# Kernel tuning notes

Measured on AMD Instinct MI355X. Metric: run time of the kernel, lower is better.

The kernel has to match this reference:

```python
import jax, jax.numpy as jnp
import numpy as np

B = 4096
NC = 64        # n_concepts
NT = 16        # n_tasks
H = 256        # prior_units (prior_layers = 1)
HID = 256      # prior_hids = [256, 256]
K = 20         # n_components
IN = 3 * NC + NT + 1        # GRU input size = 209
MLP_IN = H + 3 * NC + NT    # rnn_out input = 464
LOG_2PI = float(np.log(2.0 * np.pi))


def setup_inputs() -> dict:
    key = jax.random.key(0)
    ks = jax.random.split(key, 16)
    s = 0.05
    inp = {
        "z": jax.random.normal(ks[0], (B, NC), jnp.float32),
        "c": jax.random.normal(ks[1], (B, NC + NT), jnp.float32),
        "b": (jax.random.uniform(ks[2], (B, NC)) < 0.5).astype(jnp.float32),
        "m": (jax.random.uniform(ks[3], (B, NC)) < 0.5).astype(jnp.float32),
        # GRU (PyTorch layout: gates ordered r, z, n)
        "W_ih": jax.random.normal(ks[4], (3 * H, IN), jnp.float32) * s,
        "W_hh": jax.random.normal(ks[5], (3 * H, H), jnp.float32) * s,
        "b_ih": jax.random.normal(ks[6], (3 * H,), jnp.float32) * s,
        "b_hh": jax.random.normal(ks[7], (3 * H,), jnp.float32) * s,
        # rnn_out MLP: Linear(464,256)+Tanh, Linear(256,256)+Tanh, Linear(256,3K)
        "W1": jax.random.normal(ks[8], (HID, MLP_IN), jnp.float32) * s,
        "b1": jax.random.normal(ks[9], (HID,), jnp.float32) * s,
        "W2": jax.random.normal(ks[10], (HID, HID), jnp.float32) * s,
        "b2": jax.random.normal(ks[11], (HID,), jnp.float32) * s,
        "W3": jax.random.normal(ks[12], (3 * K, HID), jnp.float32) * s,
        "b3": jax.random.normal(ks[13], (3 * K,), jnp.float32) * s,
    }
    return inp


def _logp(z, c, b, m, W_ih, W_hh, b_ih, b_hh, W1, b1, W2, b2, W3, b3):
    Bsz, d = z.shape
    cbm = jnp.concatenate([c, b, m], axis=1)               # [B, 3*NC+NT]
    # z input at step t is -1 for t=0, else z[:, t-1]
    z_prev = jnp.concatenate(
        [-jnp.ones((Bsz, 1), z.dtype), z[:, :-1]], axis=1)  # [B, d]
    # Precompute the input-gate projections for all steps without
    # materializing the full [d, B, IN] sequence tensor:
    # column 0 of W_ih multiplies z_prev; the rest multiplies cbm.
    gi_cbm = cbm @ W_ih[:, 1:].T + b_ih                    # [B, 3H]
    gi = gi_cbm[None, :, :] + z_prev.T[:, :, None] * W_ih[:, 0][None, None, :]  # [d, B, 3H]

    def gru_step(h, gi_t):
        gh = h @ W_hh.T + b_hh
        gi_r, gi_u, gi_n = jnp.split(gi_t, 3, axis=-1)
        gh_r, gh_u, gh_n = jnp.split(gh, 3, axis=-1)
        r = jax.nn.sigmoid(gi_r + gh_r)
        u = jax.nn.sigmoid(gi_u + gh_u)
        n = jnp.tanh(gi_n + r * gh_n)
        h_new = (1.0 - u) * n + u * h
        return h_new, h_new

    h0 = jnp.zeros((Bsz, W_hh.shape[1]), z.dtype)
    _, hs = jax.lax.scan(gru_step, h0, gi)                 # [d, B, H]
    hs = jnp.transpose(hs, (1, 0, 2))                      # [B, d, H]

    feat = jnp.concatenate(
        [hs, jnp.broadcast_to(cbm[:, None, :], (Bsz, d, cbm.shape[1]))],
        axis=2)                                            # [B, d, MLP_IN]
    h1 = jnp.tanh(feat @ W1.T + b1)
    h2 = jnp.tanh(h1 @ W2.T + b2)
    params = h2 @ W3.T + b3                                # [B, d, 3K]

    logits, means, lsigmas = jnp.split(params, 3, axis=-1)
    t = z[..., None]                                       # [B, d, 1]
    log_norm = -lsigmas - 0.5 * LOG_2PI
    diff = (t - means) * jnp.exp(-lsigmas)
    log_kernel = -0.5 * jnp.square(diff)
    log_like = (jax.nn.logsumexp(log_kernel + log_norm + logits, axis=-1)
                - jax.nn.logsumexp(logits, axis=-1))       # [B, d]

    query = m * (1.0 - b)
    mask = jnp.sort(query, axis=1)[:, ::-1]                # descending sort of values
    return jnp.sum(log_like * mask, axis=1)                # [B]


def reference(z, c, b, m, W_ih, W_hh, b_ih, b_hh, W1, b1, W2, b2, W3, b3):
    return _logp(z, c, b, m, W_ih, W_hh, b_ih, b_hh,
                 W1, b1, W2, b2, W3, b3)
```

## Files before the change

kernel.cpp:

```cpp
#include <hip/hip_runtime.h>
#include <hip/hip_bf16.h>

#define BATCH  4096
#define NCC    64
#define HDIM   256
#define G3     768
#define NROW   (BATCH*NCC)
#define NK     20
#define LOG2PI 1.8378770664093453f

typedef __attribute__((ext_vector_type(8))) short bf16x8;
typedef __attribute__((ext_vector_type(4))) float f32x4;

__device__ __forceinline__ float sigm(float x) { return 1.0f/(1.0f + __expf(-x)); }
__device__ __forceinline__ float tanh_fast(float x) { return 1.0f - 2.0f/(__expf(2.0f*x) + 1.0f); }
__device__ __forceinline__ unsigned short f2bf(float x) {
  __hip_bfloat16 h = __float2bfloat16(x);
  return __builtin_bit_cast(unsigned short, h);
}

__global__ __launch_bounds__(256) void k_cvtall(
    const float* __restrict__ c, const float* __restrict__ bv,
    const float* __restrict__ mv, const float* __restrict__ W_ih,
    const float* __restrict__ W_hh, const float* __restrict__ W1,
    const float* __restrict__ W2, const float* __restrict__ W3,
    unsigned short* __restrict__ cbmB, unsigned short* __restrict__ CW,
    unsigned short* __restrict__ WhhB, unsigned short* __restrict__ W1aB,
    unsigned short* __restrict__ W2B, unsigned short* __restrict__ W3pB,
    float* __restrict__ w0) {
  int idx = blockIdx.x*256 + threadIdx.x;
  if (idx < 1048576) {
    int row = idx >> 8, k = idx & 255;
    float v = 0.f;
    if (k < 80)       v = c [row*80 + k];
    else if (k < 144) v = bv[row*64 + (k-80)];
    else if (k < 208) v = mv[row*64 + (k-144)];
    cbmB[idx] = f2bf(v);
    return;
  }
  idx -= 1048576;
  if (idx < 262144) {
    int n = idx >> 8, k = idx & 255;
    float v = 0.f;
    if (n < 768) { if (k < 208) v = W_ih[n*209 + 1 + k]; }
    else         { if (k < 208) v = W1[(n-768)*464 + 256 + k]; }
    CW[idx] = f2bf(v);
    return;
  }
  idx -= 262144;
  if (idx < 196608) { WhhB[idx] = f2bf(W_hh[idx]); return; }
  idx -= 196608;
  if (idx < 65536) { int n = idx>>8, k = idx&255; W1aB[idx] = f2bf(W1[n*464+k]); return; }
  idx -= 65536;
  if (idx < 65536) { W2B[idx] = f2bf(W2[idx]); return; }
  idx -= 65536;
  if (idx < 16384) {
    int n = idx >> 8;
    float v = 0.f;
    if (n < 60) v = W3[idx];
    W3pB[idx] = f2bf(v);
    return;
  }
  idx -= 16384;
  if (idx < 768) w0[idx] = W_ih[idx*209];
}

__global__ __launch_bounds__(512) void k_pre(
    const unsigned short* __restrict__ A, const unsigned short* __restrict__ Bw,
    const float* __restrict__ b_ih, const float* __restrict__ b_hh,
    const float* __restrict__ b1,
    float* __restrict__ gi, float* __restrict__ P1) {
  __shared__ __align__(16) unsigned short As[128*64];
  __shared__ __align__(16) unsigned short Bs[128*64];
  int tid = threadIdx.x;
  int rb = blockIdx.x >> 3, cb = blockIdx.x & 7;
  long row0 = (long)rb * 128;
  int n0 = cb * 128;
  int wv = tid >> 6, lane = tid & 63;
  int lq = lane >> 4, l16 = lane & 15;
  int wrg = wv & 3, wcg = wv >> 2;
  f32x4 acc[2][4];
#pragma unroll
  for (int i = 0; i < 2; ++i)
#pragma unroll
    for (int j = 0; j < 4; ++j) acc[i][j] = (f32x4){0.f,0.f,0.f,0.f};
  for (int kb = 0; kb < 256; kb += 64) {
#pragma unroll
    for (int i = 0; i < 2; ++i) {
      int s = i*512 + tid;
      int r = s >> 3, cg = (s & 7) ^ (r & 7);
      *(uint4*)&As[s*8] = *(const uint4*)&A[(row0 + r)*256 + kb + cg*8];
      *(uint4*)&Bs[s*8] = *(const uint4*)&Bw[(long)(n0 + r)*256 + kb + cg*8];
    }
    __syncthreads();
#pragma unroll
    for (int kc = 0; kc < 2; ++kc) {
      int csel = kc*4 + lq;
      bf16x8 af[2];
#pragma unroll
      for (int rt = 0; rt < 2; ++rt) {
        int r = wrg*32 + rt*16 + l16;
        af[rt] = *(const bf16x8*)&As[r*64 + ((csel ^ (r & 7)))*8];
      }
#pragma unroll
      for (int ct = 0; ct < 4; ++ct) {
        int n = wcg*64 + ct*16 + l16;
        bf16x8 bfr = *(const bf16x8*)&Bs[n*64 + ((csel ^ (n & 7)))*8];
        acc[0][ct] = __builtin_amdgcn_mfma_f32_16x16x32_bf16(af[0], bfr, acc[0][ct], 0, 0, 0);
        acc[1][ct] = __builtin_amdgcn_mfma_f32_16x16x32_bf16(af[1], bfr, acc[1][ct], 0, 0, 0);
      }
    }
    __syncthreads();
  }
#pragma unroll
  for (int rt = 0; rt < 2; ++rt)
#pragma unroll
    for (int q = 0; q < 4; ++q) {
      long row = row0 + wrg*32 + rt*16 + lq*4 + q;
#pragma unroll
      for (int ct = 0; ct < 4; ++ct) {
        int n = n0 + wcg*64 + ct*16 + l16;
        float v = acc[rt][ct][q];
        if (n < 512)      gi[row*G3 + n] = v + b_ih[n] + b_hh[n];
        else if (n < 768) gi[row*G3 + n] = v + b_ih[n];
        else              P1[row*256 + (n-768)] = v + b1[n-768];
      }
    }
}

__global__ __launch_bounds__(512, 2) void k_gru(
    const float* __restrict__ z, const float* __restrict__ gi,
    const unsigned short* __restrict__ WhhB, const float* __restrict__ b_hh,
    const float* __restrict__ w0, unsigned short* __restrict__ hs) {
  __shared__ __align__(16) unsigned short hbf[16*256];
  __shared__ float hf[16*260];
  __shared__ __align__(16) float gis[16*772];
  int tid = threadIdx.x;
  int wv = tid >> 6, lane = tid & 63;
  int lq = lane >> 4, l16 = lane & 15;
  int row0 = blockIdx.x * 16;
  bf16x8 wf[6][8];
#pragma unroll
  for (int g = 0; g < 3; ++g)
#pragma unroll
    for (int tt = 0; tt < 2; ++tt)
#pragma unroll
      for (int ks = 0; ks < 8; ++ks) {
        int gcol = g*256 + wv*32 + tt*16 + l16;
        wf[g*2+tt][ks] = *(const bf16x8*)&WhhB[(long)gcol*256 + ks*32 + lq*8];
      }
  float w0v[6], bhn[2];
#pragma unroll
  for (int g = 0; g < 3; ++g)
#pragma unroll
    for (int tt = 0; tt < 2; ++tt)
      w0v[g*2+tt] = w0[g*256 + wv*32 + tt*16 + l16];
#pragma unroll
  for (int tt = 0; tt < 2; ++tt)
    bhn[tt] = b_hh[512 + wv*32 + tt*16 + l16];
  for (int s = tid; s < 16*192; s += 512) {
    int r = s / 192, c4 = (s - r*192) * 4;
    *(float4*)&gis[r*772 + c4] = *(const float4*)&gi[(long)(row0 + r)*G3 + c4];
  }
  for (int i = tid; i < 16*256; i += 512) hbf[i] = 0;
  for (int i = tid; i < 16*260; i += 512) hf[i] = 0.0f;
  __syncthreads();
#pragma unroll 1
  for (int t = 0; t < NCC; ++t) {
    f32x4 acc[6];
#pragma unroll
    for (int i = 0; i < 6; ++i) acc[i] = (f32x4){0.f,0.f,0.f,0.f};
#pragma unroll
    for (int ks = 0; ks < 8; ++ks) {
      int r = l16;
      int chunk = ks*4 + lq;
      bf16x8 af = *(const bf16x8*)&hbf[r*256 + ((chunk ^ (r & 7)))*8];
#pragma unroll
      for (int f = 0; f < 6; ++f)
        acc[f] = __builtin_amdgcn_mfma_f32_16x16x32_bf16(af, wf[f][ks], acc[f], 0, 0, 0);
    }
    __syncthreads();
    int tm = (t > 0) ? (t - 1) : 0;
    float zp[4];
#pragma unroll
    for (int q = 0; q < 4; ++q) {
      int row = row0 + lq*4 + q;
      float zv = z[row*64 + tm];
      zp[q] = (t == 0) ? -1.0f : zv;
    }
#pragma unroll
    for (int tt = 0; tt < 2; ++tt) {
      int hc = wv*32 + tt*16 + l16;
#pragma unroll
      for (int q = 0; q < 4; ++q) {
        int lrow = lq*4 + q;
        const float* gr = gis + lrow*772;
        float rr = sigm(gr[hc]       + zp[q]*w0v[tt]   + acc[tt][q]);
        float uu = sigm(gr[256+hc]   + zp[q]*w0v[2+tt] + acc[2+tt][q]);
        float nn = tanh_fast(gr[512+hc] + zp[q]*w0v[4+tt] + rr*(acc[4+tt][q] + bhn[tt]));
        float hp = hf[lrow*260 + hc];
        float hn = (1.0f - uu)*nn + uu*hp;
        hf[lrow*260 + hc] = hn;
        unsigned short hb = f2bf(hn);
        hbf[lrow*256 + ((hc >> 3) ^ (lrow & 7))*8 + (hc & 7)] = hb;
        hs[((long)(row0 + lrow)*64 + t)*256 + hc] = hb;
      }
    }
    __syncthreads();
  }
}

__global__ __launch_bounds__(512) void k_l1(
    const unsigned short* __restrict__ A, const unsigned short* __restrict__ Bw,
    const float* __restrict__ P1, unsigned short* __restrict__ Out) {
  __shared__ __align__(16) unsigned short As[128*64];
  __shared__ __align__(16) unsigned short Bs[256*64];
  int tid = threadIdx.x;
  long row0 = (long)blockIdx.x * 128;
  int wv = tid >> 6, lane = tid & 63;
  int lq = lane >> 4, l16 = lane & 15;
  int wrg = wv & 3, wcg = wv >> 2;
  f32x4 acc[2][8];
#pragma unroll
  for (int i = 0; i < 2; ++i)
#pragma unroll
    for (int j = 0; j < 8; ++j) acc[i][j] = (f32x4){0.f,0.f,0.f,0.f};
  for (int kb = 0; kb < 256; kb += 64) {
#pragma unroll
    for (int i = 0; i < 2; ++i) {
      int s = i*512 + tid;
      int r = s >> 3, cg = (s & 7) ^ (r & 7);
      *(uint4*)&As[s*8] = *(const uint4*)&A[(row0 + r)*256 + kb + cg*8];
    }
#pragma unroll
    for (int i = 0; i < 4; ++i) {
      int s = i*512 + tid;
      int r = s >> 3, cg = (s & 7) ^ (r & 7);
      *(uint4*)&Bs[s*8] = *(const uint4*)&Bw[(long)r*256 + kb + cg*8];
    }
    __syncthreads();
#pragma unroll
    for (int kc = 0; kc < 2; ++kc) {
      int csel = kc*4 + lq;
      bf16x8 af[2];
#pragma unroll
      for (int rt = 0; rt < 2; ++rt) {
        int r = wrg*32 + rt*16 + l16;
        af[rt] = *(const bf16x8*)&As[r*64 + ((csel ^ (r & 7)))*8];
      }
#pragma unroll
      for (int ct = 0; ct < 8; ++ct) {
        int n = wcg*128 + ct*16 + l16;
        bf16x8 bfr = *(const bf16x8*)&Bs[n*64 + ((csel ^ (n & 7)))*8];
        acc[0][ct] = __builtin_amdgcn_mfma_f32_16x16x32_bf16(af[0], bfr, acc[0][ct], 0, 0, 0);
        acc[1][ct] = __builtin_amdgcn_mfma_f32_16x16x32_bf16(af[1], bfr, acc[1][ct], 0, 0, 0);
      }
    }
    __syncthreads();
  }
#pragma unroll
  for (int rt = 0; rt < 2; ++rt)
#pragma unroll
    for (int q = 0; q < 4; ++q) {
      long row = row0 + wrg*32 + rt*16 + lq*4 + q;
#pragma unroll
      for (int ct = 0; ct < 8; ++ct) {
        int n = wcg*128 + ct*16 + l16;
        float b = P1[(row >> 6)*256 + n];
        Out[row*256 + n] = f2bf(tanh_fast(acc[rt][ct][q] + b));
      }
    }
}

__global__ __launch_bounds__(512) void k_l23(
    const unsigned short* __restrict__ A, const unsigned short* __restrict__ W2B,
    const float* __restrict__ b2, const unsigned short* __restrict__ W3pB,
    const float* __restrict__ b3, const float* __restrict__ z,
    float* __restrict__ ll) {
  __shared__ __align__(16) unsigned short As[128*64];
  __shared__ __align__(16) unsigned short Bs[256*64];
  __shared__ __align__(16) unsigned short h2s[128*256];
  int tid = threadIdx.x;
  long row0 = (long)blockIdx.x * 128;
  int wv = tid >> 6, lane = tid & 63;
  int lq = lane >> 4, l16 = lane & 15;
  int wrg = wv & 3, wcg = wv >> 2;
  f32x4 acc[2][8];
#pragma unroll
  for (int i = 0; i < 2; ++i)
#pragma unroll
    for (int j = 0; j < 8; ++j) acc[i][j] = (f32x4){0.f,0.f,0.f,0.f};
  for (int kb = 0; kb < 256; kb += 64) {
#pragma unroll
    for (int i = 0; i < 2; ++i) {
      int s = i*512 + tid;
      int r = s >> 3, cg = (s & 7) ^ (r & 7);
      *(uint4*)&As[s*8] = *(const uint4*)&A[(row0 + r)*256 + kb + cg*8];
    }
#pragma unroll
    for (int i = 0; i < 4; ++i) {
      int s = i*512 + tid;
      int r = s >> 3, cg = (s & 7) ^ (r & 7);
      *(uint4*)&Bs[s*8] = *(const uint4*)&W2B[(long)r*256 + kb + cg*8];
    }
    __syncthreads();
#pragma unroll
    for (int kc = 0; kc < 2; ++kc) {
      int csel = kc*4 + lq;
      bf16x8 af[2];
#pragma unroll
      for (int rt = 0; rt < 2; ++rt) {
        int r = wrg*32 + rt*16 + l16;
        af[rt] = *(const bf16x8*)&As[r*64 + ((csel ^ (r & 7)))*8];
      }
#pragma unroll
      for (int ct = 0; ct < 8; ++ct) {
        int n = wcg*128 + ct*16 + l16;
        bf16x8 bfr = *(const bf16x8*)&Bs[n*64 + ((csel ^ (n & 7)))*8];
        acc[0][ct] = __builtin_amdgcn_mfma_f32_16x16x32_bf16(af[0], bfr, acc[0][ct], 0, 0, 0);
        acc[1][ct] = __builtin_amdgcn_mfma_f32_16x16x32_bf16(af[1], bfr, acc[1][ct], 0, 0, 0);
      }
    }
    __syncthreads();
  }
#pragma unroll
  for (int rt = 0; rt < 2; ++rt)
#pragma unroll
    for (int q = 0; q < 4; ++q) {
      int lr = wrg*32 + rt*16 + lq*4 + q;
#pragma unroll
      for (int ct = 0; ct < 8; ++ct) {
        int n = wcg*128 + ct*16 + l16;
        h2s[lr*256 + ((n >> 3) ^ (lr & 7))*8 + (n & 7)] =
            f2bf(tanh_fast(acc[rt][ct][q] + b2[n]));
      }
    }
#pragma unroll
  for (int i = 0; i < 4; ++i) {
    int s = i*512 + tid;
    int r = s >> 5, cc = s & 31, cg = cc ^ (r & 7);
    *(uint4*)&Bs[r*256 + cg*8] = *(const uint4*)&W3pB[r*256 + cc*8];
  }
  __syncthreads();
  f32x4 pacc[4];
#pragma unroll
  for (int j = 0; j < 4; ++j) pacc[j] = (f32x4){0.f,0.f,0.f,0.f};
#pragma unroll
  for (int ks = 0; ks < 8; ++ks) {
    int chunk = ks*4 + lq;
    int ar = wv*16 + l16;
    bf16x8 af = *(const bf16x8*)&h2s[ar*256 + ((chunk ^ (ar & 7)))*8];
#pragma unroll
    for (int ct = 0; ct < 4; ++ct) {
      int br = ct*16 + l16;
      bf16x8 bfr = *(const bf16x8*)&Bs[br*256 + ((chunk ^ (br & 7)))*8];
      pacc[ct] = __builtin_amdgcn_mfma_f32_16x16x32_bf16(af, bfr, pacc[ct], 0, 0, 0);
    }
  }
  float* Ps = (float*)&h2s[wv*16*256];
#pragma unroll
  for (int ct = 0; ct < 4; ++ct) {
    int n = ct*16 + l16;
    float b = (n < 60) ? b3[n] : 0.0f;
#pragma unroll
    for (int q = 0; q < 4; ++q)
      Ps[(lq*4 + q)*68 + n] = pacc[ct][q] + b;
  }
  if (lane < 16) {
    long grow = row0 + wv*16 + lane;
    float zv = z[grow];
    const float* p = &Ps[lane*68];
    float mx1 = -1e30f;
#pragma unroll
    for (int i = 0; i < NK; ++i) mx1 = fmaxf(mx1, p[i]);
    float s1 = 0.0f;
#pragma unroll
    for (int i = 0; i < NK; ++i) s1 += __expf(p[i] - mx1);
    float lse1 = mx1 + __logf(s1);
    float a[NK];
    float mx2 = -1e30f;
#pragma unroll
    for (int i = 0; i < NK; ++i) {
      float lg = p[i], me = p[20+i], ls = p[40+i];
      float e = __expf(-ls);
      float d = (zv - me) * e;
      float ai = -0.5f*d*d - ls - 0.5f*LOG2PI + lg;
      a[i] = ai;
      mx2 = fmaxf(mx2, ai);
    }
    float s2 = 0.0f;
#pragma unroll
    for (int i = 0; i < NK; ++i) s2 += __expf(a[i] - mx2);
    float lse2 = mx2 + __logf(s2);
    ll[grow] = lse2 - lse1;
  }
}

__global__ __launch_bounds__(256) void k_final(const float* __restrict__ bv,
    const float* __restrict__ mv, const float* __restrict__ ll,
    float* __restrict__ out) {
  int tid = threadIdx.x;
  int wave = tid >> 6, lane = tid & 63;
  int b = blockIdx.x*4 + wave;
  float q = mv[b*64 + lane] * (1.0f - bv[b*64 + lane]);
  unsigned long long bal = __ballot(q > 0.5f);
  int S = __popcll(bal);
  float val = (lane < S) ? ll[(long)b*64 + lane] : 0.0f;
#pragma unroll
  for (int off = 32; off > 0; off >>= 1) val += __shfl_down(val, off);
  if (lane == 0) out[b] = val;
}

extern "C" void kernel_launch(void* const* d_in, const int* in_sizes, int n_in,
                              void* d_out, int out_size, void* d_ws, size_t ws_size,
                              hipStream_t stream) {
  const float* z    = (const float*)d_in[0];
  const float* c    = (const float*)d_in[1];
  const float* bv   = (const float*)d_in[2];
  const float* mv   = (const float*)d_in[3];
  const float* W_ih = (const float*)d_in[4];
  const float* W_hh = (const float*)d_in[5];
  const float* b_ih = (const float*)d_in[6];
  const float* b_hh = (const float*)d_in[7];
  const float* W1   = (const float*)d_in[8];
  const float* b1   = (const float*)d_in[9];
  const float* W2   = (const float*)d_in[10];
  const float* b2   = (const float*)d_in[11];
  const float* W3   = (const float*)d_in[12];
  const float* b3   = (const float*)d_in[13];
  float* out = (float*)d_out;

  char* p = (char*)d_ws;
  auto alloc = [&](size_t bytes) {
    char* q = p;
    p += (bytes + 255) & ~(size_t)255;
    return q;
  };
  unsigned short* cbmB = (unsigned short*)alloc((size_t)BATCH*256*2);
  unsigned short* CW   = (unsigned short*)alloc((size_t)1024*256*2);
  unsigned short* WhhB = (unsigned short*)alloc((size_t)G3*256*2);
  unsigned short* W1aB = (unsigned short*)alloc((size_t)256*256*2);
  unsigned short* W2B  = (unsigned short*)alloc((size_t)256*256*2);
  unsigned short* W3pB = (unsigned short*)alloc((size_t)64*256*2);
  float* w0 = (float*)alloc((size_t)G3*4);
  float* gi = (float*)alloc((size_t)BATCH*G3*4);
  float* P1 = (float*)alloc((size_t)BATCH*256*4);
  float* ll = (float*)alloc((size_t)NROW*4);
  unsigned short* hs = (unsigned short*)alloc((size_t)NROW*HDIM*2);

  k_cvtall<<<6468, 256, 0, stream>>>(c, bv, mv, W_ih, W_hh, W1, W2, W3,
                                     cbmB, CW, WhhB, W1aB, W2B, W3pB, w0);
  k_pre<<<256, 512, 0, stream>>>(cbmB, CW, b_ih, b_hh, b1, gi, P1);
  k_gru<<<256, 512, 0, stream>>>(z, gi, WhhB, b_hh, w0, hs);
  k_l1<<<NROW/128, 512, 0, stream>>>(hs, W1aB, P1, hs);
  k_l23<<<NROW/128, 512, 0, stream>>>(hs, W2B, b2, W3pB, b3, z, ll);
  k_final<<<BATCH/4, 256, 0, stream>>>(bv, mv, ll, out);
}
```

Baseline: 528.8 us.

## Widen GRU to 1024 threads and fuse MLP layers into one kernel

The GRU kernel now uses 16 waves, each owning 16 hidden columns, and keeps the previous hidden state in registers instead of LDS. Gate biases are folded into the MFMA accumulator init, z is staged in LDS, and the hs global write is deferred and coalesced from LDS. The two MLP kernels are merged into one k_mlp working on 64-row blocks, so h1 stays in LDS and never round-trips through global memory. The costs are more LDS per MLP block, a 64-row tile that reuses the W1/W2 tiles less, and a modified swizzle.

```diff
diff --git a/kernel.cpp b/kernel.cpp
--- a/kernel.cpp
+++ b/kernel.cpp
@@ -18,6 +18,7 @@
   __hip_bfloat16 h = __float2bfloat16(x);
   return __builtin_bit_cast(unsigned short, h);
 }
+__device__ __forceinline__ int swz(int r) { return (r & 7) ^ ((r & 8) >> 2); }
 
 __global__ __launch_bounds__(256) void k_cvtall(
     const float* __restrict__ c, const float* __restrict__ bv,
@@ -128,248 +129,226 @@
     }
 }
 
-__global__ __launch_bounds__(512, 2) void k_gru(
+__global__ __launch_bounds__(1024) void k_gru(
     const float* __restrict__ z, const float* __restrict__ gi,
     const unsigned short* __restrict__ WhhB, const float* __restrict__ b_hh,
     const float* __restrict__ w0, unsigned short* __restrict__ hs) {
   __shared__ __align__(16) unsigned short hbf[16*256];
-  __shared__ float hf[16*260];
   __shared__ __align__(16) float gis[16*772];
+  __shared__ __align__(16) float zs[64*16];
   int tid = threadIdx.x;
   int wv = tid >> 6, lane = tid & 63;
   int lq = lane >> 4, l16 = lane & 15;
   int row0 = blockIdx.x * 16;
-  bf16x8 wf[6][8];
+  int hc = wv*16 + l16;
+  bf16x8 wf[3][8];
 #pragma unroll
   for (int g = 0; g < 3; ++g)
 #pragma unroll
-    for (int tt = 0; tt < 2; ++tt)
-#pragma unroll
-      for (int ks = 0; ks < 8; ++ks) {
-        int gcol = g*256 + wv*32 + tt*16 + l16;
-        wf[g*2+tt][ks] = *(const bf16x8*)&WhhB[(long)gcol*256 + ks*32 + lq*8];
-      }
-  float w0v[6], bhn[2];
-#pragma unroll
-  for (int g = 0; g < 3; ++g)
-#pragma unroll
-    for (int tt = 0; tt < 2; ++tt)
-      w0v[g*2+tt] = w0[g*256 + wv*32 + tt*16 + l16];
-#pragma unroll
-  for (int tt = 0; tt < 2; ++tt)
-    bhn[tt] = b_hh[512 + wv*32 + tt*16 + l16];
-  for (int s = tid; s < 16*192; s += 512) {
-    int r = s / 192, c4 = (s - r*192) * 4;
-    *(float4*)&gis[r*772 + c4] = *(const float4*)&gi[(long)(row0 + r)*G3 + c4];
-  }
-  for (int i = tid; i < 16*256; i += 512) hbf[i] = 0;
-  for (int i = tid; i < 16*260; i += 512) hf[i] = 0.0f;
+    for (int ks = 0; ks < 8; ++ks)
+      wf[g][ks] = *(const bf16x8*)&WhhB[(long)(g*256 + hc)*256 + ks*32 + lq*8];
+  float w0r = w0[hc], w0u = w0[256+hc], w0n = w0[512+hc];
+  float bhn = b_hh[512+hc];
+  {
+    int t = tid >> 4, r = tid & 15;
+    zs[t*16 + r] = z[(row0+r)*64 + t];
+  }
+#pragma unroll
+  for (int i = 0; i < 3; ++i) {
+    int s = i*1024 + tid;
+    int r = s / 192, c4 = (s - r*192)*4;
+    *(float4*)&gis[r*772 + c4] = *(const float4*)&gi[(long)(row0+r)*768 + c4];
+  }
+  for (int i = tid; i < 2048; i += 1024) ((unsigned int*)hbf)[i] = 0u;
+  float hp0 = 0.f, hp1 = 0.f, hp2 = 0.f, hp3 = 0.f;
+  int swzA = swz(l16);
+  const unsigned short* copysrc = &hbf[wv*256 + (((lane>>1) ^ swz(wv))*8 + (lane&1)*4)];
+  unsigned short* hsp = hs + (long)(row0 + wv)*64*256 + lane*4;
+  int wr0 = lq*4;
+  int hbw[4];
+#pragma unroll
+  for (int q = 0; q < 4; ++q) {
+    int r = wr0 + q;
+    hbw[q] = r*256 + (((hc>>3) ^ swz(r))*8 + (hc&7));
+  }
+  int gbase = wr0*772 + hc;
   __syncthreads();
 #pragma unroll 1
-  for (int t = 0; t < NCC; ++t) {
-    f32x4 acc[6];
-#pragma unroll
-    for (int i = 0; i < 6; ++i) acc[i] = (f32x4){0.f,0.f,0.f,0.f};
+  for (int t = 0; t < 64; ++t) {
+    uint2 cdat;
+    if (t) cdat = *(const uint2*)copysrc;
+    f32x4 a0, a1, a2;
+    int tm = t ? (t-1) : 0;
+    float4 zv4 = *(const float4*)&zs[tm*16 + wr0];
+    float zp[4];
+#pragma unroll
+    for (int q = 0; q < 4; ++q) {
+      zp[q] = t ? ((&zv4.x)[q]) : -1.0f;
+      a0[q] = gis[gbase + q*772]       + zp[q]*w0r;
+      a1[q] = gis[gbase + q*772 + 256] + zp[q]*w0u;
+      a2[q] = bhn;
+    }
 #pragma unroll
     for (int ks = 0; ks < 8; ++ks) {
-      int r = l16;
-      int chunk = ks*4 + lq;
-      bf16x8 af = *(const bf16x8*)&hbf[r*256 + ((chunk ^ (r & 7)))*8];
-#pragma unroll
-      for (int f = 0; f < 6; ++f)
-        acc[f] = __builtin_amdgcn_mfma_f32_16x16x32_bf16(af, wf[f][ks], acc[f], 0, 0, 0);
-    }
+      bf16x8 af = *(const bf16x8*)&hbf[l16*256 + (((ks*4+lq) ^ swzA))*8];
+      a0 = __builtin_amdgcn_mfma_f32_16x16x32_bf16(af, wf[0][ks], a0, 0, 0, 0);
+      a1 = __builtin_amdgcn_mfma_f32_16x16x32_bf16(af, wf[1][ks], a1, 0, 0, 0);
+      a2 = __builtin_amdgcn_mfma_f32_16x16x32_bf16(af, wf[2][ks], a2, 0, 0, 0);
+    }
+    if (t) *(uint2*)&hsp[(t-1)*256] = cdat;
     __syncthreads();
-    int tm = (t > 0) ? (t - 1) : 0;
-    float zp[4];
 #pragma unroll
     for (int q = 0; q < 4; ++q) {
-      int row = row0 + lq*4 + q;
-      float zv = z[row*64 + tm];
-      zp[q] = (t == 0) ? -1.0f : zv;
-    }
-#pragma unroll
-    for (int tt = 0; tt < 2; ++tt) {
-      int hc = wv*32 + tt*16 + l16;
-#pragma unroll
-      for (int q = 0; q < 4; ++q) {
-        int lrow = lq*4 + q;
-        const float* gr = gis + lrow*772;
-        float rr = sigm(gr[hc]       + zp[q]*w0v[tt]   + acc[tt][q]);
-        float uu = sigm(gr[256+hc]   + zp[q]*w0v[2+tt] + acc[2+tt][q]);
-        float nn = tanh_fast(gr[512+hc] + zp[q]*w0v[4+tt] + rr*(acc[4+tt][q] + bhn[tt]));
-        float hp = hf[lrow*260 + hc];
-        float hn = (1.0f - uu)*nn + uu*hp;
-        hf[lrow*260 + hc] = hn;
-        unsigned short hb = f2bf(hn);
-        hbf[lrow*256 + ((hc >> 3) ^ (lrow & 7))*8 + (hc & 7)] = hb;
-        hs[((long)(row0 + lrow)*64 + t)*256 + hc] = hb;
-      }
+      float rr = sigm(a0[q]);
+      float uu = sigm(a1[q]);
+      float gn = gis[gbase + q*772 + 512];
+      float nn = tanh_fast(gn + zp[q]*w0n + rr*a2[q]);
+      float hp = (q==0)?hp0:(q==1)?hp1:(q==2)?hp2:hp3;
+      float hn = uu*(hp - nn) + nn;
+      if (q==0) hp0 = hn; else if (q==1) hp1 = hn; else if (q==2) hp2 = hn; else hp3 = hn;
+      hbf[hbw[q]] = f2bf(hn);
     }
     __syncthreads();
   }
-}
-
-__global__ __launch_bounds__(512) void k_l1(
-    const unsigned short* __restrict__ A, const unsigned short* __restrict__ Bw,
-    const float* __restrict__ P1, unsigned short* __restrict__ Out) {
-  __shared__ __align__(16) unsigned short As[128*64];
+  uint2 cdat = *(const uint2*)copysrc;
+  *(uint2*)&hsp[63*256] = cdat;
+}
+
+__global__ __launch_bounds__(512) void k_mlp(
+    const unsigned short* __restrict__ hs, const unsigned short* __restrict__ W1aB,
+    const float* __restrict__ P1, const unsigned short* __restrict__ W2B,
+    const float* __restrict__ b2, const unsigned short* __restrict__ W3pB,
+    const float* __restrict__ b3, const float* __restrict__ z,
+    float* __restrict__ ll) {
+  __shared__ __align__(16) unsigned short As[64*64];
   __shared__ __align__(16) unsigned short Bs[256*64];
+  __shared__ __align__(16) unsigned short h1s[64*256];
+  __shared__ __align__(16) unsigned short h2s[64*256];
+  __shared__ float Ps[64*68];
   int tid = threadIdx.x;
-  long row0 = (long)blockIdx.x * 128;
+  int blk = blockIdx.x;
+  long row0 = (long)blk * 64;
   int wv = tid >> 6, lane = tid & 63;
   int lq = lane >> 4, l16 = lane & 15;
   int wrg = wv & 3, wcg = wv >> 2;
-  f32x4 acc[2][8];
-#pragma unroll
-  for (int i = 0; i < 2; ++i)
-#pragma unroll
-    for (int j = 0; j < 8; ++j) acc[i][j] = (f32x4){0.f,0.f,0.f,0.f};
-  for (int kb = 0; kb < 256; kb += 64) {
-#pragma unroll
-    for (int i = 0; i < 2; ++i) {
-      int s = i*512 + tid;
-      int r = s >> 3, cg = (s & 7) ^ (r & 7);
-      *(uint4*)&As[s*8] = *(const uint4*)&A[(row0 + r)*256 + kb + cg*8];
-    }
-#pragma unroll
-    for (int i = 0; i < 4; ++i) {
-      int s = i*512 + tid;
-      int r = s >> 3, cg = (s & 7) ^ (r & 7);
-      *(uint4*)&Bs[s*8] = *(const uint4*)&Bw[(long)r*256 + kb + cg*8];
-    }
-    __syncthreads();
-#pragma unroll
-    for (int kc = 0; kc < 2; ++kc) {
-      int csel = kc*4 + lq;
-      bf16x8 af[2];
-#pragma unroll
-      for (int rt = 0; rt < 2; ++rt) {
-        int r = wrg*32 + rt*16 + l16;
-        af[rt] = *(const bf16x8*)&As[r*64 + ((csel ^ (r & 7)))*8];
-      }
+  {
+    f32x4 acc[8];
+#pragma unroll
+    for (int j = 0; j < 8; ++j) acc[j] = (f32x4){0.f,0.f,0.f,0.f};
+    for (int kb = 0; kb < 256; kb += 64) {
+      {
+        int s = tid;
+        int r = s >> 3, cg = (s & 7) ^ (r & 7);
+        *(uint4*)&As[s*8] = *(const uint4*)&hs[(row0 + r)*256 + kb + cg*8];
+      }
+#pragma unroll
+      for (int i = 0; i < 4; ++i) {
+        int s = i*512 + tid;
+        int r = s >> 3, cg = (s & 7) ^ (r & 7);
+        *(uint4*)&Bs[s*8] = *(const uint4*)&W1aB[(long)r*256 + kb + cg*8];
+      }
+      __syncthreads();
+#pragma unroll
+      for (int kc = 0; kc < 2; ++kc) {
+        int csel = kc*4 + lq;
+        int ar = wrg*16 + l16;
+        bf16x8 af = *(const bf16x8*)&As[ar*64 + ((csel ^ (ar & 7)))*8];
+#pragma unroll
+        for (int ct = 0; ct < 8; ++ct) {
+          int n = wcg*128 + ct*16 + l16;
+          bf16x8 bfr = *(const bf16x8*)&Bs[n*64 + ((csel ^ (n & 7)))*8];
+          acc[ct] = __builtin_amdgcn_mfma_f32_16x16x32_bf16(af, bfr, acc[ct], 0, 0, 0);
+        }
+      }
+      __syncthreads();
+    }
+#pragma unroll
+    for (int q = 0; q < 4; ++q) {
+      int rl = wrg*16 + lq*4 + q;
 #pragma unroll
       for (int ct = 0; ct < 8; ++ct) {
         int n = wcg*128 + ct*16 + l16;
-        bf16x8 bfr = *(const bf16x8*)&Bs[n*64 + ((csel ^ (n & 7)))*8];
-        acc[0][ct] = __builtin_amdgcn_mfma_f32_16x16x32_bf16(af[0], bfr, acc[0][ct], 0, 0, 0);
-        acc[1][ct] = __builtin_amdgcn_mfma_f32_16x16x32_bf16(af[1], bfr, acc[1][ct], 0, 0, 0);
-      }
-    }
-    __syncthreads();
-  }
-#pragma unroll
-  for (int rt = 0; rt < 2; ++rt)
+        float v = tanh_fast(acc[ct][q] + P1[blk*256 + n]);
+        h1s[rl*256 + (((n>>3) ^ swz(rl))*8 + (n&7))] = f2bf(v);
+      }
+    }
+  }
+  {
+    f32x4 acc[8];
+#pragma unroll
+    for (int j = 0; j < 8; ++j) acc[j] = (f32x4){0.f,0.f,0.f,0.f};
+    for (int kb4 = 0; kb4 < 4; ++kb4) {
+#pragma unroll
+      for (int i = 0; i < 4; ++i) {
+        int s = i*512 + tid;
+        int r = s >> 3, cg = (s & 7) ^ (r & 7);
+        *(uint4*)&Bs[s*8] = *(const uint4*)&W2B[(long)r*256 + kb4*64 + cg*8];
+      }
+      __syncthreads();
+#pragma unroll
+      for (int kc = 0; kc < 2; ++kc) {
+        int csel = kc*4 + lq;
+        int cglob = kb4*8 + csel;
+        int ar = wrg*16 + l16;
+        bf16x8 af = *(const bf16x8*)&h1s[ar*256 + ((cglob ^ swz(ar)))*8];
+#pragma unroll
+        for (int ct = 0; ct < 8; ++ct) {
+          int n = wcg*128 + ct*16 + l16;
+          bf16x8 bfr = *(const bf16x8*)&Bs[n*64 + ((csel ^ (n & 7)))*8];
+          acc[ct] = __builtin_amdgcn_mfma_f32_16x16x32_bf16(af, bfr, acc[ct], 0, 0, 0);
+        }
+      }
+      __syncthreads();
+    }
 #pragma unroll
     for (int q = 0; q < 4; ++q) {
-      long row = row0 + wrg*32 + rt*16 + lq*4 + q;
+      int rl = wrg*16 + lq*4 + q;
 #pragma unroll
       for (int ct = 0; ct < 8; ++ct) {
         int n = wcg*128 + ct*16 + l16;
-        float b = P1[(row >> 6)*256 + n];
-        Out[row*256 + n] = f2bf(tanh_fast(acc[rt][ct][q] + b));
-      }
-    }
-}
-
-__global__ __launch_bounds__(512) void k_l23(
-    const unsigned short* __restrict__ A, const unsigned short* __restrict__ W2B,
-    const float* __restrict__ b2, const unsigned short* __restrict__ W3pB,
-    const float* __restrict__ b3, const float* __restrict__ z,
-    float* __restrict__ ll) {
-  __shared__ __align__(16) unsigned short As[128*64];
-  __shared__ __align__(16) unsigned short Bs[256*64];
-  __shared__ __align__(16) unsigned short h2s[128*256];
-  int tid = threadIdx.x;
-  long row0 = (long)blockIdx.x * 128;
-  int wv = tid >> 6, lane = tid & 63;
-  int lq = lane >> 4, l16 = lane & 15;
-  int wrg = wv & 3, wcg = wv >> 2;
-  f32x4 acc[2][8];
-#pragma unroll
-  for (int i = 0; i < 2; ++i)
-#pragma unroll
-    for (int j = 0; j < 8; ++j) acc[i][j] = (f32x4){0.f,0.f,0.f,0.f};
-  for (int kb = 0; kb < 256; kb += 64) {
-#pragma unroll
-    for (int i = 0; i < 2; ++i) {
-      int s = i*512 + tid;
-      int r = s >> 3, cg = (s & 7) ^ (r & 7);
-      *(uint4*)&As[s*8] = *(const uint4*)&A[(row0 + r)*256 + kb + cg*8];
-    }
-#pragma unroll
-    for (int i = 0; i < 4; ++i) {
-      int s = i*512 + tid;
-      int r = s >> 3, cg = (s & 7) ^ (r & 7);
-      *(uint4*)&Bs[s*8] = *(const uint4*)&W2B[(long)r*256 + kb + cg*8];
-    }
-    __syncthreads();
-#pragma unroll
-    for (int kc = 0; kc < 2; ++kc) {
-      int csel = kc*4 + lq;
-      bf16x8 af[2];
-#pragma unroll
-      for (int rt = 0; rt < 2; ++rt) {
-        int r = wrg*32 + rt*16 + l16;
-        af[rt] = *(const bf16x8*)&As[r*64 + ((csel ^ (r & 7)))*8];
-      }
-#pragma unroll
-      for (int ct = 0; ct < 8; ++ct) {
-        int n = wcg*128 + ct*16 + l16;
-        bf16x8 bfr = *(const bf16x8*)&Bs[n*64 + ((csel ^ (n & 7)))*8];
-        acc[0][ct] = __builtin_amdgcn_mfma_f32_16x16x32_bf16(af[0], bfr, acc[0][ct], 0, 0, 0);
-        acc[1][ct] = __builtin_amdgcn_mfma_f32_16x16x32_bf16(af[1], bfr, acc[1][ct], 0, 0, 0);
-      }
-    }
-    __syncthreads();
-  }
-#pragma unroll
-  for (int rt = 0; rt < 2; ++rt)
-#pragma unroll
-    for (int q = 0; q < 4; ++q) {
-      int lr = wrg*32 + rt*16 + lq*4 + q;
-#pragma unroll
-      for (int ct = 0; ct < 8; ++ct) {
-        int n = wcg*128 + ct*16 + l16;
-        h2s[lr*256 + ((n >> 3) ^ (lr & 7))*8 + (n & 7)] =
-            f2bf(tanh_fast(acc[rt][ct][q] + b2[n]));
-      }
-    }
+        float v = tanh_fast(acc[ct][q] + b2[n]);
+        h2s[rl*256 + (((n>>3) ^ swz(rl))*8 + (n&7))] = f2bf(v);
+      }
+    }
+  }
 #pragma unroll
   for (int i = 0; i < 4; ++i) {
     int s = i*512 + tid;
-    int r = s >> 5, cc = s & 31, cg = cc ^ (r & 7);
-    *(uint4*)&Bs[r*256 + cg*8] = *(const uint4*)&W3pB[r*256 + cc*8];
+    int r = s >> 5, cc = s & 31;
+    *(uint4*)&Bs[r*256 + ((cc ^ swz(r)))*8] = *(const uint4*)&W3pB[r*256 + cc*8];
   }
   __syncthreads();
-  f32x4 pacc[4];
-#pragma unroll
-  for (int j = 0; j < 4; ++j) pacc[j] = (f32x4){0.f,0.f,0.f,0.f};
-#pragma unroll
-  for (int ks = 0; ks < 8; ++ks) {
-    int chunk = ks*4 + lq;
-    int ar = wv*16 + l16;
-    bf16x8 af = *(const bf16x8*)&h2s[ar*256 + ((chunk ^ (ar & 7)))*8];
-#pragma unroll
-    for (int ct = 0; ct < 4; ++ct) {
-      int br = ct*16 + l16;
-      bf16x8 bfr = *(const bf16x8*)&Bs[br*256 + ((chunk ^ (br & 7)))*8];
-      pacc[ct] = __builtin_amdgcn_mfma_f32_16x16x32_bf16(af, bfr, pacc[ct], 0, 0, 0);
-    }
-  }
-  float* Ps = (float*)&h2s[wv*16*256];
-#pragma unroll
-  for (int ct = 0; ct < 4; ++ct) {
-    int n = ct*16 + l16;
-    float b = (n < 60) ? b3[n] : 0.0f;
-#pragma unroll
-    for (int q = 0; q < 4; ++q)
-      Ps[(lq*4 + q)*68 + n] = pacc[ct][q] + b;
-  }
-  if (lane < 16) {
-    long grow = row0 + wv*16 + lane;
-    float zv = z[grow];
-    const float* p = &Ps[lane*68];
+  {
+    int mt = wv & 3, np = wv >> 2;
+    f32x4 acc[2];
+#pragma unroll
+    for (int j = 0; j < 2; ++j) acc[j] = (f32x4){0.f,0.f,0.f,0.f};
+#pragma unroll
+    for (int ks = 0; ks < 8; ++ks) {
+      int csel = ks*4 + lq;
+      int ar = mt*16 + l16;
+      bf16x8 af = *(const bf16x8*)&h2s[ar*256 + ((csel ^ swz(ar)))*8];
+#pragma unroll
+      for (int j = 0; j < 2; ++j) {
+        int br = (np*2 + j)*16 + l16;
+        bf16x8 bfr = *(const bf16x8*)&Bs[br*256 + ((csel ^ swz(br)))*8];
+        acc[j] = __builtin_amdgcn_mfma_f32_16x16x32_bf16(af, bfr, acc[j], 0, 0, 0);
+      }
+    }
+#pragma unroll
+    for (int j = 0; j < 2; ++j) {
+      int n = (np*2 + j)*16 + l16;
+      float b = (n < 60) ? b3[n] : 0.0f;
+#pragma unroll
+      for (int q = 0; q < 4; ++q)
+        Ps[(mt*16 + lq*4 + q)*68 + n] = acc[j][q] + b;
+    }
+  }
+  __syncthreads();
+  if (wv < 4 && lane < 16) {
+    int rl = wv*16 + lane;
+    float zv = z[blk*64 + rl];
+    const float* p = &Ps[rl*68];
     float mx1 = -1e30f;
 #pragma unroll
     for (int i = 0; i < NK; ++i) mx1 = fmaxf(mx1, p[i]);
@@ -392,7 +371,7 @@
 #pragma unroll
     for (int i = 0; i < NK; ++i) s2 += __expf(a[i] - mx2);
     float lse2 = mx2 + __logf(s2);
-    ll[grow] = lse2 - lse1;
+    ll[row0 + rl] = lse2 - lse1;
   }
 }
 
@@ -451,8 +430,7 @@
   k_cvtall<<<6468, 256, 0, stream>>>(c, bv, mv, W_ih, W_hh, W1, W2, W3,
                                      cbmB, CW, WhhB, W1aB, W2B, W3pB, w0);
   k_pre<<<256, 512, 0, stream>>>(cbmB, CW, b_ih, b_hh, b1, gi, P1);
-  k_gru<<<256, 512, 0, stream>>>(z, gi, WhhB, b_hh, w0, hs);
-  k_l1<<<NROW/128, 512, 0, stream>>>(hs, W1aB, P1, hs);
-  k_l23<<<NROW/128, 512, 0, stream>>>(hs, W2B, b2, W3pB, b3, z, ll);
+  k_gru<<<256, 1024, 0, stream>>>(z, gi, WhhB, b_hh, w0, hs);
+  k_mlp<<<BATCH, 512, 0, stream>>>(hs, W1aB, P1, W2B, b2, W3pB, b3, z, ll);
   k_final<<<BATCH/4, 256, 0, stream>>>(bv, mv, ll, out);
 }
```

Result: slower. 700.1 us (+32.4%).

## Double-buffer GRU hidden state and coalesce hs stores via shared memory

Applied to the files above, without the earlier changes.

The GRU kernel now double-buffers the bf16 hidden state in shared memory, which removes one barrier per timestep. The fp32 previous hidden state moves into registers, and z is staged in shared memory. Gate preactivations are folded into the MFMA accumulator initialisation. The hs output is written as coalesced 16-byte rows copied from the previous step's shared buffer, replacing the scattered 2-byte global stores. The launch-bounds occupancy hint is dropped, and the MLP kernel's LDS swizzle is extended to use row bit 3 to cut bank conflicts.

```diff
diff --git a/kernel.cpp b/kernel.cpp
--- a/kernel.cpp
+++ b/kernel.cpp
@@ -18,6 +18,7 @@
   __hip_bfloat16 h = __float2bfloat16(x);
   return __builtin_bit_cast(unsigned short, h);
 }
+__device__ __forceinline__ int swz(int r) { return (r & 7) ^ ((r & 8) >> 2); }
 
 __global__ __launch_bounds__(256) void k_cvtall(
     const float* __restrict__ c, const float* __restrict__ bv,
@@ -128,13 +129,13 @@
     }
 }
 
-__global__ __launch_bounds__(512, 2) void k_gru(
+__global__ __launch_bounds__(512) void k_gru(
     const float* __restrict__ z, const float* __restrict__ gi,
     const unsigned short* __restrict__ WhhB, const float* __restrict__ b_hh,
     const float* __restrict__ w0, unsigned short* __restrict__ hs) {
-  __shared__ __align__(16) unsigned short hbf[16*256];
-  __shared__ float hf[16*260];
+  __shared__ __align__(16) unsigned short hbf[2*16*256];
   __shared__ __align__(16) float gis[16*772];
+  __shared__ __align__(16) float zs[64*16];
   int tid = threadIdx.x;
   int wv = tid >> 6, lane = tid & 63;
   int lq = lane >> 4, l16 = lane & 15;
@@ -145,10 +146,8 @@
 #pragma unroll
     for (int tt = 0; tt < 2; ++tt)
 #pragma unroll
-      for (int ks = 0; ks < 8; ++ks) {
-        int gcol = g*256 + wv*32 + tt*16 + l16;
-        wf[g*2+tt][ks] = *(const bf16x8*)&WhhB[(long)gcol*256 + ks*32 + lq*8];
-      }
+      for (int ks = 0; ks < 8; ++ks)
+        wf[g*2+tt][ks] = *(const bf16x8*)&WhhB[(long)(g*256 + wv*32 + tt*16 + l16)*256 + ks*32 + lq*8];
   float w0v[6], bhn[2];
 #pragma unroll
   for (int g = 0; g < 3; ++g)
@@ -158,56 +157,76 @@
 #pragma unroll
   for (int tt = 0; tt < 2; ++tt)
     bhn[tt] = b_hh[512 + wv*32 + tt*16 + l16];
-  for (int s = tid; s < 16*192; s += 512) {
-    int r = s / 192, c4 = (s - r*192) * 4;
-    *(float4*)&gis[r*772 + c4] = *(const float4*)&gi[(long)(row0 + r)*G3 + c4];
-  }
-  for (int i = tid; i < 16*256; i += 512) hbf[i] = 0;
-  for (int i = tid; i < 16*260; i += 512) hf[i] = 0.0f;
+  for (int i = tid; i < 1024; i += 512) {
+    int t = i >> 4, r = i & 15;
+    zs[i] = z[(row0+r)*64 + t];
+  }
+#pragma unroll
+  for (int i = 0; i < 6; ++i) {
+    int s = i*512 + tid;
+    int r = s / 192, c4 = (s - r*192)*4;
+    *(float4*)&gis[r*772 + c4] = *(const float4*)&gi[(long)(row0+r)*768 + c4];
+  }
+  for (int i = tid; i < 2048; i += 512) ((unsigned int*)hbf)[i] = 0u;
+  float hp[2][4] = {{0.f,0.f,0.f,0.f},{0.f,0.f,0.f,0.f}};
+  const int s7 = l16 & 7;
+  const int arow = l16*256;
+  const int r4 = lq*4;
+  const int cr = tid >> 5, ccc = tid & 31;
+  const int csrc = cr*256 + ((ccc ^ (cr & 7)))*8;
+  unsigned short* cbase = hs + (long)(row0+cr)*64*256 + ccc*8;
   __syncthreads();
 #pragma unroll 1
-  for (int t = 0; t < NCC; ++t) {
-    f32x4 acc[6];
-#pragma unroll
-    for (int i = 0; i < 6; ++i) acc[i] = (f32x4){0.f,0.f,0.f,0.f};
-#pragma unroll
-    for (int ks = 0; ks < 8; ++ks) {
-      int r = l16;
-      int chunk = ks*4 + lq;
-      bf16x8 af = *(const bf16x8*)&hbf[r*256 + ((chunk ^ (r & 7)))*8];
-#pragma unroll
-      for (int f = 0; f < 6; ++f)
-        acc[f] = __builtin_amdgcn_mfma_f32_16x16x32_bf16(af, wf[f][ks], acc[f], 0, 0, 0);
-    }
-    __syncthreads();
-    int tm = (t > 0) ? (t - 1) : 0;
+  for (int t = 0; t < 64; ++t) {
+    const int co = (t & 1) << 12;
+    const int no = co ^ 4096;
+    uint4 cdat;
+    if (t) cdat = *(const uint4*)&hbf[co + csrc];
     float zp[4];
-#pragma unroll
-    for (int q = 0; q < 4; ++q) {
-      int row = row0 + lq*4 + q;
-      float zv = z[row*64 + tm];
-      zp[q] = (t == 0) ? -1.0f : zv;
-    }
+    {
+      float4 zv4 = *(const float4*)&zs[(t ? (t-1) : 0)*16 + r4];
+#pragma unroll
+      for (int q = 0; q < 4; ++q) zp[q] = t ? (&zv4.x)[q] : -1.0f;
+    }
+    f32x4 a[6];
 #pragma unroll
     for (int tt = 0; tt < 2; ++tt) {
       int hc = wv*32 + tt*16 + l16;
 #pragma unroll
       for (int q = 0; q < 4; ++q) {
-        int lrow = lq*4 + q;
-        const float* gr = gis + lrow*772;
-        float rr = sigm(gr[hc]       + zp[q]*w0v[tt]   + acc[tt][q]);
-        float uu = sigm(gr[256+hc]   + zp[q]*w0v[2+tt] + acc[2+tt][q]);
-        float nn = tanh_fast(gr[512+hc] + zp[q]*w0v[4+tt] + rr*(acc[4+tt][q] + bhn[tt]));
-        float hp = hf[lrow*260 + hc];
-        float hn = (1.0f - uu)*nn + uu*hp;
-        hf[lrow*260 + hc] = hn;
-        unsigned short hb = f2bf(hn);
-        hbf[lrow*256 + ((hc >> 3) ^ (lrow & 7))*8 + (hc & 7)] = hb;
-        hs[((long)(row0 + lrow)*64 + t)*256 + hc] = hb;
-      }
-    }
-    __syncthreads();
-  }
+        a[tt][q]   = gis[(r4+q)*772 + hc]       + zp[q]*w0v[tt];
+        a[2+tt][q] = gis[(r4+q)*772 + 256 + hc] + zp[q]*w0v[2+tt];
+        a[4+tt][q] = bhn[tt];
+      }
+    }
+#pragma unroll
+    for (int ks = 0; ks < 8; ++ks) {
+      bf16x8 af = *(const bf16x8*)&hbf[co + arow + (((ks*4+lq) ^ s7))*8];
+#pragma unroll
+      for (int f = 0; f < 6; ++f)
+        a[f] = __builtin_amdgcn_mfma_f32_16x16x32_bf16(af, wf[f][ks], a[f], 0, 0, 0);
+    }
+    if (t) *(uint4*)(cbase + (t-1)*256) = cdat;
+#pragma unroll
+    for (int tt = 0; tt < 2; ++tt) {
+      int hc = wv*32 + tt*16 + l16;
+      int hchunk = hc >> 3, hlow = hc & 7;
+#pragma unroll
+      for (int q = 0; q < 4; ++q) {
+        int r = r4 + q;
+        float rr = sigm(a[tt][q]);
+        float uu = sigm(a[2+tt][q]);
+        float gn = gis[r*772 + 512 + hc];
+        float nn = tanh_fast(gn + zp[q]*w0v[4+tt] + rr*a[4+tt][q]);
+        float hn = uu*(hp[tt][q] - nn) + nn;
+        hp[tt][q] = hn;
+        hbf[no + r*256 + ((hchunk ^ (r & 7)))*8 + hlow] = f2bf(hn);
+      }
+    }
+    __syncthreads();
+  }
+  uint4 cdat = *(const uint4*)&hbf[0 + csrc];
+  *(uint4*)(cbase + 63*256) = cdat;
 }
 
 __global__ __launch_bounds__(512) void k_l1(
@@ -331,15 +350,15 @@
 #pragma unroll
       for (int ct = 0; ct < 8; ++ct) {
         int n = wcg*128 + ct*16 + l16;
-        h2s[lr*256 + ((n >> 3) ^ (lr & 7))*8 + (n & 7)] =
+        h2s[lr*256 + (((n >> 3) ^ swz(lr))*8 + (n & 7))] =
             f2bf(tanh_fast(acc[rt][ct][q] + b2[n]));
       }
     }
 #pragma unroll
   for (int i = 0; i < 4; ++i) {
     int s = i*512 + tid;
-    int r = s >> 5, cc = s & 31, cg = cc ^ (r & 7);
-    *(uint4*)&Bs[r*256 + cg*8] = *(const uint4*)&W3pB[r*256 + cc*8];
+    int r = s >> 5, cc = s & 31;
+    *(uint4*)&Bs[r*256 + ((cc ^ swz(r)))*8] = *(const uint4*)&W3pB[r*256 + cc*8];
   }
   __syncthreads();
   f32x4 pacc[4];
@@ -349,11 +368,11 @@
   for (int ks = 0; ks < 8; ++ks) {
     int chunk = ks*4 + lq;
     int ar = wv*16 + l16;
-    bf16x8 af = *(const bf16x8*)&h2s[ar*256 + ((chunk ^ (ar & 7)))*8];
+    bf16x8 af = *(const bf16x8*)&h2s[ar*256 + ((chunk ^ swz(ar)))*8];
 #pragma unroll
     for (int ct = 0; ct < 4; ++ct) {
       int br = ct*16 + l16;
-      bf16x8 bfr = *(const bf16x8*)&Bs[br*256 + ((chunk ^ (br & 7)))*8];
+      bf16x8 bfr = *(const bf16x8*)&Bs[br*256 + ((chunk ^ swz(br)))*8];
       pacc[ct] = __builtin_amdgcn_mfma_f32_16x16x32_bf16(af, bfr, pacc[ct], 0, 0, 0);
     }
   }
```

Measured after the change: 631.7 us. 1.19x slower.
